# Kernel tuning notes

Measured on AMD Instinct MI355X. Metric: run time of the kernel, lower is better.

## Reference

```python
import jax, jax.numpy as jnp
import numpy as np

N = 100000
E = 3200000
IN_F = 128
OUT_F = 64
ALPHA = 0.1  # leaky relu negative slope


def spmm(rows, cols, vals, X):
    # sparse [N,N] (COO) @ dense [N,F] -> [N,F]
    return jax.ops.segment_sum(vals[:, None] * X[cols], rows, num_segments=N)


def setup_inputs() -> dict:
    key = jax.random.key(0)
    ks = jax.random.split(key, 16)
    d = {
        "x": jax.random.normal(ks[0], (N, IN_F), dtype=jnp.float32),
        "W": jax.random.normal(ks[1], (IN_F, OUT_F), dtype=jnp.float32) * (1.414 / np.sqrt(IN_F)),
        "a": jax.random.normal(ks[2], (2 * OUT_F, 1), dtype=jnp.float32) * 0.1,
    }
    names = ["A", "P1", "P2", "P3"]
    for i, nm in enumerate(names):
        d[nm + "_rows"] = jax.random.randint(ks[3 + 3 * i], (E,), 0, N, dtype=jnp.int32)
        d[nm + "_cols"] = jax.random.randint(ks[4 + 3 * i], (E,), 0, N, dtype=jnp.int32)
        d[nm + "_vals"] = jax.random.uniform(ks[5 + 3 * i], (E,), dtype=jnp.float32) / 32.0
    return d


def reference(x, W, a, A_rows, A_cols, A_vals,
              P1_rows, P1_cols, P1_vals,
              P2_rows, P2_cols, P2_vals,
              P3_rows, P3_cols, P3_vals):
    support0 = x @ W                         # [N, F]
    h_A = spmm(A_rows, A_cols, A_vals, support0)
    h_A2 = spmm(A_rows, A_cols, A_vals, h_A)
    h_A3 = spmm(A_rows, A_cols, A_vals, h_A2)
    h_sct1 = jnp.abs(spmm(P1_rows, P1_cols, P1_vals, support0))
    h_sct2 = jnp.abs(spmm(P2_rows, P2_cols, P2_vals, support0))
    h_sct3 = jnp.abs(spmm(P3_rows, P3_cols, P3_vals, support0))

    h = support0
    F2 = 2 * OUT_F
    # faithful to torch: cat along dim0 then raw row-major view(N, 1, 2F)
    def pair(hk):
        return jnp.concatenate([h, hk], axis=0).reshape(N, 1, F2)

    a_input = jnp.concatenate(
        [pair(h_A), pair(h_A2), pair(h_A3), pair(h_sct1), pair(h_sct2), pair(h_sct3)],
        axis=1,
    ).reshape(N, 6, F2)
    e = jax.nn.leaky_relu((a_input @ a)[..., 0], negative_slope=ALPHA)  # [N, 6]
    attention = jax.nn.softmax(e, axis=1).reshape(N, 6, 1)
    # faithful to torch: cat along dim2 -> [N,F,6], then raw view(N,6,F)
    h_all = jnp.stack([h_A, h_A2, h_A3, h_sct1, h_sct2, h_sct3], axis=2).reshape(N, 6, OUT_F)
    h_prime = jnp.mean(attention * h_all, axis=1)  # [N, F]
    return (h_prime, attention)
```

## Files before the change

### kernel.cpp

```cpp
#include <hip/hip_runtime.h>
#include <math.h>

#define NN 100000
#define EE 3200000
#define INF 128
#define OUTF 64
#define ALPHA 0.1f

#define BROWS 128
#define NBINS 782
#define CAP 4472
#define SCHUNK 4096
#define NCH 2
#define SBLK (SCHUNK * NCH)
#define NSUM ((NBINS + 3) / 4)

#define GR 64
#define XPAD 132

__device__ __forceinline__ unsigned short f2bf(float f)
{
    unsigned u = __float_as_uint(f);
    u += 0x7FFFu + ((u >> 16) & 1u);
    return (unsigned short)(u >> 16);
}
__device__ __forceinline__ float bf2f(unsigned short b)
{
    return __uint_as_float((unsigned)b << 16);
}

__global__ __launch_bounds__(256) void gemm_kernel(
    const float* __restrict__ x, const float* __restrict__ W,
    unsigned short* __restrict__ outbf)
{
    __shared__ float Wl[INF * OUTF];
    __shared__ float xL[GR * XPAD];

    int tid = threadIdx.x;
    int tx = tid & 15;
    int ty = tid >> 4;
    int r0 = blockIdx.x * GR;

    const float4* W4 = (const float4*)W;
    float4* Wl4 = (float4*)Wl;
    for (int i = tid; i < INF * OUTF / 4; i += 256) Wl4[i] = W4[i];

    for (int i = tid; i < GR * (INF / 4); i += 256) {
        int row = i >> 5;
        int c4 = i & 31;
        int gr = r0 + row;
        float4 v = make_float4(0.f, 0.f, 0.f, 0.f);
        if (gr < NN) v = *(const float4*)&x[(size_t)gr * INF + 4 * c4];
        *(float4*)&xL[row * XPAD + 4 * c4] = v;
    }
    __syncthreads();

    float acc[4][4];
#pragma unroll
    for (int i = 0; i < 4; i++)
#pragma unroll
        for (int j = 0; j < 4; j++) acc[i][j] = 0.f;

#pragma unroll 4
    for (int k4 = 0; k4 < INF / 4; k4++) {
        float4 xv[4], wv[4];
#pragma unroll
        for (int i = 0; i < 4; i++)
            xv[i] = *(float4*)&xL[(4 * ty + i) * XPAD + 4 * k4];
#pragma unroll
        for (int kk = 0; kk < 4; kk++)
            wv[kk] = *(float4*)&Wl[(4 * k4 + kk) * OUTF + 4 * tx];
#pragma unroll
        for (int i = 0; i < 4; i++) {
#pragma unroll
            for (int kk = 0; kk < 4; kk++) {
                acc[i][0] = fmaf(((float*)&xv[i])[kk], ((float*)&wv[kk])[0], acc[i][0]);
                acc[i][1] = fmaf(((float*)&xv[i])[kk], ((float*)&wv[kk])[1], acc[i][1]);
                acc[i][2] = fmaf(((float*)&xv[i])[kk], ((float*)&wv[kk])[2], acc[i][2]);
                acc[i][3] = fmaf(((float*)&xv[i])[kk], ((float*)&wv[kk])[3], acc[i][3]);
            }
        }
    }

#pragma unroll
    for (int i = 0; i < 4; i++) {
        int gr = r0 + 4 * ty + i;
        if (gr < NN) {
            uint2 o;
            o.x = (unsigned)f2bf(acc[i][0]) | ((unsigned)f2bf(acc[i][1]) << 16);
            o.y = (unsigned)f2bf(acc[i][2]) | ((unsigned)f2bf(acc[i][3]) << 16);
            *(uint2*)&outbf[(size_t)gr * OUTF + 4 * tx] = o;
        }
    }
}

__global__ __launch_bounds__(256) void bin_scatter4(
    const int* __restrict__ rows0, const int* __restrict__ cols0, const float* __restrict__ vals0,
    const int* __restrict__ rows1, const int* __restrict__ cols1, const float* __restrict__ vals1,
    const int* __restrict__ rows2, const int* __restrict__ cols2, const float* __restrict__ vals2,
    const int* __restrict__ rows3, const int* __restrict__ cols3, const float* __restrict__ vals3,
    int* __restrict__ gcur_all,
    uint2* __restrict__ b0, uint2* __restrict__ b1,
    uint2* __restrict__ b2, uint2* __restrict__ b3)
{
    __shared__ uint2 rec[SCHUNK];
    __shared__ int hc[NCH][NBINS];
    __shared__ int lcur[NBINS];
    __shared__ int off[NBINS + 1];
    __shared__ int cur[NBINS];
    __shared__ int sums[NSUM];

    int m = blockIdx.y;
    const int* rows; const int* cols; const float* vals; uint2* binned;
    if (m == 0)      { rows = rows0; cols = cols0; vals = vals0; binned = b0; }
    else if (m == 1) { rows = rows1; cols = cols1; vals = vals1; binned = b1; }
    else if (m == 2) { rows = rows2; cols = cols2; vals = vals2; binned = b2; }
    else             { rows = rows3; cols = cols3; vals = vals3; binned = b3; }
    int* gcur = gcur_all + m * NBINS;

    int tid = threadIdx.x;
    int base = blockIdx.x * SBLK;
    int n = min(SBLK, EE - base);
    if (n <= 0) return;

    for (int i = tid; i < NCH * NBINS; i += 256) ((int*)hc)[i] = 0;
    __syncthreads();
    for (int i = tid; i < n; i += 256) {
        int r = rows[base + i];
        atomicAdd(&hc[i >> 12][r >> 7], 1);
    }
    __syncthreads();
    for (int b = tid; b < NBINS; b += 256) {
        int c = hc[0][b] + hc[1][b];
        lcur[b] = c ? atomicAdd(&gcur[b], c) : 0;
    }

    for (int cc = 0; cc < NCH; cc++) {
        int c0 = cc * SCHUNK;
        if (c0 >= n) break;
        int nc = min(SCHUNK, n - c0);
        __syncthreads();
        if (tid < NSUM) {
            int s = 0;
#pragma unroll
            for (int k = 0; k < 4; k++) { int b = 4 * tid + k; if (b < NBINS) s += hc[cc][b]; }
            sums[tid] = s;
        }
        __syncthreads();
        if (tid == 0) {
            int acc = 0;
            for (int t = 0; t < NSUM; t++) { int v = sums[t]; sums[t] = acc; acc += v; }
            off[NBINS] = acc;
        }
        __syncthreads();
        if (tid < NSUM) {
            int acc = sums[tid];
#pragma unroll
            for (int k = 0; k < 4; k++) {
                int b = 4 * tid + k;
                if (b < NBINS) { off[b] = acc; cur[b] = acc; acc += hc[cc][b]; }
            }
        }
        __syncthreads();
        for (int i = tid; i < nc; i += 256) {
            int r = rows[base + c0 + i];
            int ccol = cols[base + c0 + i];
            float v = vals[base + c0 + i];
            int b = r >> 7;
            int pos = atomicAdd(&cur[b], 1);
            uint2 q;
            q.x = (unsigned)ccol | ((unsigned)(r & (BROWS - 1)) << 17)
                | ((unsigned)(b & 0xFF) << 24);
            q.y = __float_as_uint(v);
            rec[pos] = q;
        }
        __syncthreads();
        for (int i = tid; i < nc; i += 256) {
            uint2 q = rec[i];
            int b = (int)(q.x >> 24);
            if (b + 768 < NBINS && off[b + 768] <= i) b += 768;
            else if (b + 512 < NBINS && off[b + 512] <= i) b += 512;
            else if (b + 256 < NBINS && off[b + 256] <= i) b += 256;
            int slot = lcur[b] + (i - off[b]);
            if (slot < CAP) binned[(size_t)b * CAP + slot] = q;
        }
        __syncthreads();
        for (int b = tid; b < NBINS; b += 256) lcur[b] += hc[cc][b];
    }
}

__global__ __launch_bounds__(256) void bin_sort4(
    uint2* __restrict__ b0, uint2* __restrict__ b1,
    uint2* __restrict__ b2, uint2* __restrict__ b3,
    const int* __restrict__ gcur_all,
    int* __restrict__ rowptr_all, int* __restrict__ cnt_all)
{
    __shared__ uint2 rin[CAP];
    __shared__ uint2 rout[CAP];
    __shared__ int h[BROWS], hs[BROWS], cur[BROWS];

    int m = blockIdx.y;
    uint2* binned = (m == 0) ? b0 : (m == 1) ? b1 : (m == 2) ? b2 : b3;
    const int* gcur = gcur_all + m * NBINS;
    int* rowptr = rowptr_all + m * NN;
    int* cnt = cnt_all + m * NN;

    int bin = blockIdx.x;
    int tid = threadIdx.x;
    int c = min(gcur[bin], CAP);
    uint2* src = binned + (size_t)bin * CAP;

    for (int i = tid; i < c; i += 256) rin[i] = src[i];
    if (tid < BROWS) h[tid] = 0;
    __syncthreads();
    for (int i = tid; i < c; i += 256)
        atomicAdd(&h[(rin[i].x >> 17) & (BROWS - 1)], 1);
    __syncthreads();
    if (tid < BROWS) hs[tid] = h[tid];
    __syncthreads();
#pragma unroll
    for (int o = 1; o < BROWS; o <<= 1) {
        int w = (tid >= o && tid < BROWS) ? hs[tid - o] : 0;
        __syncthreads();
        if (tid < BROWS) hs[tid] += w;
        __syncthreads();
    }
    if (tid < BROWS) cur[tid] = hs[tid] - h[tid];
    __syncthreads();
    for (int i = tid; i < c; i += 256) {
        uint2 q = rin[i];
        int pos = atomicAdd(&cur[(q.x >> 17) & (BROWS - 1)], 1);
        rout[pos] = q;
    }
    __syncthreads();
    for (int i = tid; i < c; i += 256) src[i] = rout[i];

    if (tid < BROWS) {
        int gr = bin * BROWS + tid;
        if (gr < NN) {
            rowptr[gr] = bin * CAP + (hs[tid] - h[tid]);
            cnt[gr] = h[tid];
        }
    }
}

__device__ __forceinline__ void spmm_row(
    const int* __restrict__ rowptr, const int* __restrict__ cnt,
    const uint2* __restrict__ edges,
    const unsigned short* __restrict__ Xb, unsigned short* __restrict__ Yb)
{
    int row = blockIdx.x * 4 + (threadIdx.x >> 6);
    int lane = threadIdx.x & 63;
    if (row >= NN) return;
    int s = __builtin_amdgcn_readfirstlane(rowptr[row]);
    int e = s + __builtin_amdgcn_readfirstlane(cnt[row]);
    float acc = 0.f;
    int i = s;
    for (; i + 7 < e; i += 8) {
        uint2 p0 = edges[i + 0], p1 = edges[i + 1], p2 = edges[i + 2], p3 = edges[i + 3];
        uint2 p4 = edges[i + 4], p5 = edges[i + 5], p6 = edges[i + 6], p7 = edges[i + 7];
        unsigned short x0 = Xb[(size_t)(p0.x & 0x1FFFF) * OUTF + lane];
        unsigned short x1 = Xb[(size_t)(p1.x & 0x1FFFF) * OUTF + lane];
        unsigned short x2 = Xb[(size_t)(p2.x & 0x1FFFF) * OUTF + lane];
        unsigned short x3 = Xb[(size_t)(p3.x & 0x1FFFF) * OUTF + lane];
        unsigned short x4 = Xb[(size_t)(p4.x & 0x1FFFF) * OUTF + lane];
        unsigned short x5 = Xb[(size_t)(p5.x & 0x1FFFF) * OUTF + lane];
        unsigned short x6 = Xb[(size_t)(p6.x & 0x1FFFF) * OUTF + lane];
        unsigned short x7 = Xb[(size_t)(p7.x & 0x1FFFF) * OUTF + lane];
        acc = fmaf(__uint_as_float(p0.y), bf2f(x0), acc);
        acc = fmaf(__uint_as_float(p1.y), bf2f(x1), acc);
        acc = fmaf(__uint_as_float(p2.y), bf2f(x2), acc);
        acc = fmaf(__uint_as_float(p3.y), bf2f(x3), acc);
        acc = fmaf(__uint_as_float(p4.y), bf2f(x4), acc);
        acc = fmaf(__uint_as_float(p5.y), bf2f(x5), acc);
        acc = fmaf(__uint_as_float(p6.y), bf2f(x6), acc);
        acc = fmaf(__uint_as_float(p7.y), bf2f(x7), acc);
    }
    for (; i < e; i++) {
        uint2 p = edges[i];
        acc = fmaf(__uint_as_float(p.y),
                   bf2f(Xb[(size_t)(p.x & 0x1FFFF) * OUTF + lane]), acc);
    }
    Yb[(size_t)row * OUTF + lane] = f2bf(acc);
}

__global__ __launch_bounds__(256) void spmm_csr(
    const int* __restrict__ rowptr, const int* __restrict__ cnt,
    const uint2* __restrict__ edges,
    const unsigned short* __restrict__ Xb, unsigned short* __restrict__ Yb)
{
    spmm_row(rowptr, cnt, edges, Xb, Yb);
}

__global__ __launch_bounds__(256) void spmm4(
    const int* __restrict__ rowptr_all, const int* __restrict__ cnt_all,
    const uint2* __restrict__ b0, const uint2* __restrict__ b1,
    const uint2* __restrict__ b2, const uint2* __restrict__ b3,
    const unsigned short* __restrict__ sup,
    unsigned short* __restrict__ hA, unsigned short* __restrict__ s1,
    unsigned short* __restrict__ s2, unsigned short* __restrict__ s3)
{
    int m = blockIdx.y;
    const uint2* edges = (m == 0) ? b0 : (m == 1) ? b1 : (m == 2) ? b2 : b3;
    unsigned short* out = (m == 0) ? hA : (m == 1) ? s1 : (m == 2) ? s2 : s3;
    spmm_row(rowptr_all + m * NN, cnt_all + m * NN, edges, sup, out);
}

__global__ __launch_bounds__(256) void fuse_kernel(
    const unsigned short* __restrict__ hA, const unsigned short* __restrict__ hA2,
    const unsigned short* __restrict__ hA3,
    const unsigned short* __restrict__ s1, const unsigned short* __restrict__ s2,
    const unsigned short* __restrict__ s3,
    const float* __restrict__ a, float* __restrict__ out)
{
    __shared__ float chl[4][6][OUTF];
    int wid = threadIdx.x >> 6;
    int lane = threadIdx.x & 63;
    int i = blockIdx.x * 4 + wid;
    if (i >= NN) return;

    const unsigned short* bufs[6] = {hA, hA2, hA3, s1, s2, s3};

#pragma unroll
    for (int k = 0; k < 6; k++) {
        float v = bf2f(bufs[k][(size_t)i * OUTF + lane]);
        if (k >= 3) v = fabsf(v);
        chl[wid][k][lane] = v;
    }

    float att[6];
    if (i < NN / 2) {
#pragma unroll
        for (int k = 0; k < 6; k++) att[k] = 1.0f / 6.0f;
    } else {
        int m = 2 * i - NN;
        float alo = a[lane];
        float ahi = a[64 + lane];
        float e[6];
#pragma unroll
        for (int k = 0; k < 6; k++) {
            float v0 = bf2f(bufs[k][(size_t)m * OUTF + lane]);
            float v1 = bf2f(bufs[k][(size_t)(m + 1) * OUTF + lane]);
            if (k >= 3) { v0 = fabsf(v0); v1 = fabsf(v1); }
            float p = alo * v0 + ahi * v1;
#pragma unroll
            for (int off = 32; off; off >>= 1) p += __shfl_xor(p, off);
            e[k] = (p > 0.f) ? p : ALPHA * p;
        }
        float mx = e[0];
#pragma unroll
        for (int k = 1; k < 6; k++) mx = fmaxf(mx, e[k]);
        float s = 0.f;
#pragma unroll
        for (int k = 0; k < 6; k++) { att[k] = __expf(e[k] - mx); s += att[k]; }
        float inv = 1.f / s;
#pragma unroll
        for (int k = 0; k < 6; k++) att[k] *= inv;
    }

    if (lane < 6) out[(size_t)NN * OUTF + (size_t)i * 6 + lane] = att[lane];

    float hp = 0.f;
#pragma unroll
    for (int j = 0; j < 6; j++) {
        int g = j * 64 + lane;
        hp += att[j] * chl[wid][g % 6][g / 6];
    }
    out[(size_t)i * OUTF + lane] = hp * (1.0f / 6.0f);
}

extern "C" void kernel_launch(void* const* d_in, const int* in_sizes, int n_in,
                              void* d_out, int out_size, void* d_ws, size_t ws_size,
                              hipStream_t stream)
{
    const float* x = (const float*)d_in[0];
    const float* W = (const float*)d_in[1];
    const float* a = (const float*)d_in[2];
    const int*   A_rows  = (const int*)d_in[3];
    const int*   A_cols  = (const int*)d_in[4];
    const float* A_vals  = (const float*)d_in[5];
    const int*   P1_rows = (const int*)d_in[6];
    const int*   P1_cols = (const int*)d_in[7];
    const float* P1_vals = (const float*)d_in[8];
    const int*   P2_rows = (const int*)d_in[9];
    const int*   P2_cols = (const int*)d_in[10];
    const float* P2_vals = (const float*)d_in[11];
    const int*   P3_rows = (const int*)d_in[12];
    const int*   P3_cols = (const int*)d_in[13];
    const float* P3_vals = (const float*)d_in[14];

    const size_t NF = (size_t)NN * OUTF;
    const size_t BINSZ = (size_t)NBINS * CAP;

    char* p = (char*)d_ws;
    uint2* b1 = (uint2*)p;              p += BINSZ * sizeof(uint2);
    uint2* b2 = (uint2*)p;              p += BINSZ * sizeof(uint2);
    uint2* b3 = (uint2*)p;              p += BINSZ * sizeof(uint2);
    unsigned short* bf_sup = (unsigned short*)p;  p += NF * 2;
    unsigned short* bf_hA  = (unsigned short*)p;  p += NF * 2;
    unsigned short* bf_hA2 = (unsigned short*)p;  p += NF * 2;
    unsigned short* bf_s1  = (unsigned short*)p;  p += NF * 2;
    unsigned short* bf_s2  = (unsigned short*)p;  p += NF * 2;
    unsigned short* bf_s3  = (unsigned short*)p;  p += NF * 2;
    int* gcur   = (int*)p;              p += (size_t)4 * NBINS * sizeof(int);
    int* rowptr = (int*)p;              p += (size_t)4 * NN * sizeof(int);
    int* cnt    = (int*)p;              p += (size_t)4 * NN * sizeof(int);

    uint2* b0 = (uint2*)d_out;

    const int GB = (EE + SBLK - 1) / SBLK;
    const int RB = (NN + 3) / 4;

    hipMemsetAsync(gcur, 0, (size_t)4 * NBINS * sizeof(int), stream);

    gemm_kernel<<<(NN + GR - 1) / GR, 256, 0, stream>>>(x, W, bf_sup);

    bin_scatter4<<<dim3(GB, 4), 256, 0, stream>>>(
        A_rows, A_cols, A_vals, P1_rows, P1_cols, P1_vals,
        P2_rows, P2_cols, P2_vals, P3_rows, P3_cols, P3_vals,
        gcur, b0, b1, b2, b3);

    bin_sort4<<<dim3(NBINS, 4), 256, 0, stream>>>(b0, b1, b2, b3, gcur, rowptr, cnt);

    spmm4<<<dim3(RB, 4), 256, 0, stream>>>(rowptr, cnt, b0, b1, b2, b3,
                                           bf_sup, bf_hA, bf_s1, bf_s2, bf_s3);

    spmm_csr<<<RB, 256, 0, stream>>>(rowptr, cnt, b0, bf_hA,  bf_hA2);
    spmm_csr<<<RB, 256, 0, stream>>>(rowptr, cnt, b0, bf_hA2, bf_sup);

    fuse_kernel<<<RB, 256, 0, stream>>>(bf_hA, bf_hA2, bf_sup,
                                        bf_s1, bf_s2, bf_s3, a, (float*)d_out);
}
```

Baseline: 752.7 us.

## Vectorize SpMM gathers across edge groups and parallelize scatter prefix scan

The SpMM row kernel now splits each wavefront into four groups of 16 lanes. Each lane loads 4 bf16 features (8 bytes) per edge, so one wavefront processes 8 edges per iteration, and the partial sums are reduced with cross-lane shuffles. This replaces one 2-byte gather per lane per edge, cutting gather instruction count and the serial per-edge latency chain. The binning scatter also uses smaller chunks (2048×4), and its single-thread serial prefix sum over bins becomes a parallel Hillis-Steele scan in shared memory, which adds extra barriers.

```diff
diff --git a/kernel.cpp b/kernel.cpp
--- a/kernel.cpp
+++ b/kernel.cpp
@@ -10,8 +10,8 @@
 #define BROWS 128
 #define NBINS 782
 #define CAP 4472
-#define SCHUNK 4096
-#define NCH 2
+#define SCHUNK 2048
+#define NCH 4
 #define SBLK (SCHUNK * NCH)
 #define NSUM ((NBINS + 3) / 4)
 
@@ -109,6 +109,7 @@
     __shared__ int off[NBINS + 1];
     __shared__ int cur[NBINS];
     __shared__ int sums[NSUM];
+    __shared__ int ssc[256];
 
     int m = blockIdx.y;
     const int* rows; const int* cols; const float* vals; uint2* binned;
@@ -127,11 +128,11 @@
     __syncthreads();
     for (int i = tid; i < n; i += 256) {
         int r = rows[base + i];
-        atomicAdd(&hc[i >> 12][r >> 7], 1);
+        atomicAdd(&hc[i >> 11][r >> 7], 1);
     }
     __syncthreads();
     for (int b = tid; b < NBINS; b += 256) {
-        int c = hc[0][b] + hc[1][b];
+        int c = hc[0][b] + hc[1][b] + hc[2][b] + hc[3][b];
         lcur[b] = c ? atomicAdd(&gcur[b], c) : 0;
     }
 
@@ -147,10 +148,18 @@
             sums[tid] = s;
         }
         __syncthreads();
-        if (tid == 0) {
-            int acc = 0;
-            for (int t = 0; t < NSUM; t++) { int v = sums[t]; sums[t] = acc; acc += v; }
-            off[NBINS] = acc;
+        {
+            int sv = (tid < NSUM) ? sums[tid] : 0;
+            ssc[tid] = sv;
+            __syncthreads();
+            for (int o = 1; o < 256; o <<= 1) {
+                int w = (tid >= o) ? ssc[tid - o] : 0;
+                __syncthreads();
+                ssc[tid] += w;
+                __syncthreads();
+            }
+            if (tid < NSUM) sums[tid] = ssc[tid] - sv;
+            if (tid == 255) off[NBINS] = ssc[255];
         }
         __syncthreads();
         if (tid < NSUM) {
@@ -252,36 +261,41 @@
     int row = blockIdx.x * 4 + (threadIdx.x >> 6);
     int lane = threadIdx.x & 63;
     if (row >= NN) return;
-    int s = __builtin_amdgcn_readfirstlane(rowptr[row]);
-    int e = s + __builtin_amdgcn_readfirstlane(cnt[row]);
-    float acc = 0.f;
-    int i = s;
-    for (; i + 7 < e; i += 8) {
-        uint2 p0 = edges[i + 0], p1 = edges[i + 1], p2 = edges[i + 2], p3 = edges[i + 3];
-        uint2 p4 = edges[i + 4], p5 = edges[i + 5], p6 = edges[i + 6], p7 = edges[i + 7];
-        unsigned short x0 = Xb[(size_t)(p0.x & 0x1FFFF) * OUTF + lane];
-        unsigned short x1 = Xb[(size_t)(p1.x & 0x1FFFF) * OUTF + lane];
-        unsigned short x2 = Xb[(size_t)(p2.x & 0x1FFFF) * OUTF + lane];
-        unsigned short x3 = Xb[(size_t)(p3.x & 0x1FFFF) * OUTF + lane];
-        unsigned short x4 = Xb[(size_t)(p4.x & 0x1FFFF) * OUTF + lane];
-        unsigned short x5 = Xb[(size_t)(p5.x & 0x1FFFF) * OUTF + lane];
-        unsigned short x6 = Xb[(size_t)(p6.x & 0x1FFFF) * OUTF + lane];
-        unsigned short x7 = Xb[(size_t)(p7.x & 0x1FFFF) * OUTF + lane];
-        acc = fmaf(__uint_as_float(p0.y), bf2f(x0), acc);
-        acc = fmaf(__uint_as_float(p1.y), bf2f(x1), acc);
-        acc = fmaf(__uint_as_float(p2.y), bf2f(x2), acc);
-        acc = fmaf(__uint_as_float(p3.y), bf2f(x3), acc);
-        acc = fmaf(__uint_as_float(p4.y), bf2f(x4), acc);
-        acc = fmaf(__uint_as_float(p5.y), bf2f(x5), acc);
-        acc = fmaf(__uint_as_float(p6.y), bf2f(x6), acc);
-        acc = fmaf(__uint_as_float(p7.y), bf2f(x7), acc);
-    }
-    for (; i < e; i++) {
-        uint2 p = edges[i];
-        acc = fmaf(__uint_as_float(p.y),
-                   bf2f(Xb[(size_t)(p.x & 0x1FFFF) * OUTF + lane]), acc);
-    }
-    Yb[(size_t)row * OUTF + lane] = f2bf(acc);
+    int s = rowptr[row];
+    int e = s + cnt[row];
+    int g = lane >> 4;
+    int fg = lane & 15;
+    const uint2* X4 = (const uint2*)Xb;
+
+    float a0 = 0.f, a1 = 0.f, a2 = 0.f, a3 = 0.f;
+    for (int i = s; i < e; i += 8) {
+        int ia = i + g, ib = i + 4 + g;
+        uint2 qa = make_uint2(0u, 0u), qb = make_uint2(0u, 0u);
+        if (ia < e) qa = edges[ia];
+        if (ib < e) qb = edges[ib];
+        uint2 xa = X4[(size_t)(qa.x & 0x1FFFF) * 16 + fg];
+        uint2 xb = X4[(size_t)(qb.x & 0x1FFFF) * 16 + fg];
+        float va = __uint_as_float(qa.y);
+        float vb = __uint_as_float(qb.y);
+        a0 = fmaf(va, bf2f((unsigned short)(xa.x & 0xFFFF)), a0);
+        a1 = fmaf(va, bf2f((unsigned short)(xa.x >> 16)), a1);
+        a2 = fmaf(va, bf2f((unsigned short)(xa.y & 0xFFFF)), a2);
+        a3 = fmaf(va, bf2f((unsigned short)(xa.y >> 16)), a3);
+        a0 = fmaf(vb, bf2f((unsigned short)(xb.x & 0xFFFF)), a0);
+        a1 = fmaf(vb, bf2f((unsigned short)(xb.x >> 16)), a1);
+        a2 = fmaf(vb, bf2f((unsigned short)(xb.y & 0xFFFF)), a2);
+        a3 = fmaf(vb, bf2f((unsigned short)(xb.y >> 16)), a3);
+    }
+    a0 += __shfl_xor(a0, 16); a0 += __shfl_xor(a0, 32);
+    a1 += __shfl_xor(a1, 16); a1 += __shfl_xor(a1, 32);
+    a2 += __shfl_xor(a2, 16); a2 += __shfl_xor(a2, 32);
+    a3 += __shfl_xor(a3, 16); a3 += __shfl_xor(a3, 32);
+    if (lane < 16) {
+        uint2 o;
+        o.x = (unsigned)f2bf(a0) | ((unsigned)f2bf(a1) << 16);
+        o.y = (unsigned)f2bf(a2) | ((unsigned)f2bf(a3) << 16);
+        *(uint2*)&Yb[(size_t)row * OUTF + fg * 4] = o;
+    }
 }
 
 __global__ __launch_bounds__(256) void spmm_csr(
```

After: 833.8 us. 1.11x slower.
